# Optimization experiments

Hardware: AMD Instinct MI355X
Metric: run time of the kernel (lower is better)

Reference implementation:

```python
import jax, jax.numpy as jnp
import numpy as np

N_LAYERS = 32
HIDDEN = 1024
INTER = 2816
BATCH = 256
INIT_SCALE = 0.02


def setup_inputs() -> dict:
    key = jax.random.key(0)
    k_h, k_g, k_u, k_d = jax.random.split(key, 4)
    down_std = INIT_SCALE / np.sqrt(2 * N_LAYERS)
    h = jax.random.normal(k_h, (BATCH, N_LAYERS, HIDDEN), dtype=jnp.float32)
    # torch Linear weight layout: (out_features, in_features); stack over experts
    Wg = jax.random.normal(k_g, (N_LAYERS, INTER, HIDDEN), dtype=jnp.float32) * INIT_SCALE
    Wu = jax.random.normal(k_u, (N_LAYERS, INTER, HIDDEN), dtype=jnp.float32) * INIT_SCALE
    Wd = jax.random.normal(k_d, (N_LAYERS, HIDDEN, INTER), dtype=jnp.float32) * down_std
    return {"h": h, "Wg": Wg, "Wu": Wu, "Wd": Wd}


def reference(h, Wg, Wu, Wd):
    # h: (B, N, D); Wg/Wu: (N, I, D); Wd: (N, D, I)
    gate = jnp.einsum("bnd,nid->bni", h, Wg)
    up = jnp.einsum("bnd,nid->bni", h, Wu)
    act = jax.nn.silu(gate) * up            # (B, N, I)
    out = jnp.einsum("bni,ndi->bnd", act, Wd)  # (B, N, D)
    return out
```

## Files before the change

### kernel.cpp

```cpp
#include <hip/hip_runtime.h>
#include <hip/hip_bf16.h>

#define BATCH   256
#define NLAYERS 32
#define HID     1024
#define INTER   2816
#define BK      64

typedef __attribute__((ext_vector_type(8))) short bf16x8;
typedef __attribute__((ext_vector_type(4))) float f32x4;
typedef __attribute__((ext_vector_type(4))) int   i32x4;

__device__ __forceinline__ ushort f2bf(float f) {
  __hip_bfloat16 b = __float2bfloat16(f);
  return *reinterpret_cast<ushort*>(&b);
}

__device__ __forceinline__ bf16x8 cvt8(f32x4 a, f32x4 b) {
  bf16x8 o;
  o[0] = (short)f2bf(a[0]); o[1] = (short)f2bf(a[1]);
  o[2] = (short)f2bf(a[2]); o[3] = (short)f2bf(a[3]);
  o[4] = (short)f2bf(b[0]); o[5] = (short)f2bf(b[1]);
  o[6] = (short)f2bf(b[2]); o[7] = (short)f2bf(b[3]);
  return o;
}

__global__ __launch_bounds__(256) void k_pack(
    const float* __restrict__ h, ushort* __restrict__ Xp) {
  const int r    = blockIdx.x * 4 + (threadIdx.x >> 6);
  const int lane = threadIdx.x & 63;
  const int ro   = ((r & 31) * 256 + (r >> 5)) * 1024;
  const float* src = h + (size_t)r * 1024 + lane * 4;
  ushort* dst      = Xp + ro + lane * 4;
#pragma unroll
  for (int g = 0; g < 4; ++g) {
    f32x4 v = *(const f32x4*)(src + g * 256);
    ushort4 o;
    o.x = f2bf(v[0]); o.y = f2bf(v[1]); o.z = f2bf(v[2]); o.w = f2bf(v[3]);
    *(ushort4*)(dst + g * 256) = o;
  }
}

__global__ __launch_bounds__(512) void k_gateup(
    const ushort* __restrict__ Xp, const float* __restrict__ Wg,
    const float* __restrict__ Wu, ushort* __restrict__ act) {
  const int bid   = blockIdx.x;
  const int layer = bid / (INTER / 32);
  const int it    = bid % (INTER / 32);
  const int i0    = it * 32;
  const int tid   = threadIdx.x;
  const int lane  = tid & 63;
  const int wave  = tid >> 6;
  const int m0    = wave * 32;

  __shared__ ushort lds[BATCH * BK + 64 * BK];
  ushort* Al = lds;
  ushort* Wl = lds + BATCH * BK;

  f32x4 acc[2][4] = {};

  int aldst[4];
  const ushort* asrc[4];
#pragma unroll
  for (int r = 0; r < 4; ++r) {
    int g = tid + 512 * r;
    int arow = g >> 3, akc = g & 7;
    aldst[r] = arow * BK + ((akc ^ (arow & 7)) << 3);
    asrc[r] = Xp + ((size_t)layer * BATCH + arow) * HID + akc * 8;
  }
  const int wrow = tid >> 3, wsl = tid & 7;
  const int wldst = wrow * BK + ((wsl ^ (wrow & 7)) << 3);
  const float* wsrc = (wrow < 32 ? Wg + (size_t)(i0 + wrow) * HID
                                 : Wu + (size_t)(i0 + wrow - 32) * HID) +
                      (size_t)layer * INTER * HID + wsl * 8;

  i32x4 ra[4];
  f32x4 rw[2];
#pragma unroll
  for (int r = 0; r < 4; ++r) ra[r] = *(const i32x4*)asrc[r];
  rw[0] = *(const f32x4*)wsrc; rw[1] = *(const f32x4*)(wsrc + 4);

  const int r16 = lane & 15;
  const int g4  = lane >> 4;

  const int NK = HID / BK;
  for (int k = 0; k < NK; ++k) {
    __syncthreads();
#pragma unroll
    for (int r = 0; r < 4; ++r) *(i32x4*)&Al[aldst[r]] = ra[r];
    *(bf16x8*)&Wl[wldst] = cvt8(rw[0], rw[1]);
    __syncthreads();

    if (k + 1 < NK) {
      int off = (k + 1) * BK;
#pragma unroll
      for (int r = 0; r < 4; ++r) ra[r] = *(const i32x4*)(asrc[r] + off);
      rw[0] = *(const f32x4*)(wsrc + off); rw[1] = *(const f32x4*)(wsrc + off + 4);
    }

#pragma unroll
    for (int ks = 0; ks < 2; ++ks) {
      const int kg = ks * 4 + g4;
      bf16x8 af[2];
#pragma unroll
      for (int m = 0; m < 2; ++m) {
        int row = m0 + m * 16 + r16;
        af[m] = *(bf16x8*)&Al[row * BK + ((kg ^ (row & 7)) << 3)];
      }
#pragma unroll
      for (int n = 0; n < 4; ++n) {
        int row = n * 16 + r16;
        bf16x8 bw = *(bf16x8*)&Wl[row * BK + ((kg ^ (row & 7)) << 3)];
#pragma unroll
        for (int m = 0; m < 2; ++m)
          acc[m][n] = __builtin_amdgcn_mfma_f32_16x16x32_bf16(af[m], bw, acc[m][n], 0, 0, 0);
      }
    }
  }

  const int r4 = (lane >> 4) * 4;
#pragma unroll
  for (int m = 0; m < 2; ++m)
#pragma unroll
    for (int n = 0; n < 2; ++n)
#pragma unroll
      for (int r = 0; r < 4; ++r) {
        float g = acc[m][n][r];
        float u = acc[m][n + 2][r];
        float a = (g / (1.f + __expf(-g))) * u;
        int b = m0 + m * 16 + r4 + r;
        int i = i0 + n * 16 + r16;
        act[((size_t)layer * BATCH + b) * INTER + i] = f2bf(a);
      }
}

__global__ __launch_bounds__(512) void k_down(
    const ushort* __restrict__ act, const float* __restrict__ Wd,
    float* __restrict__ out) {
  const int bid   = blockIdx.x;
  const int layer = bid / (HID / 64);
  const int dtile = bid % (HID / 64);
  const int d0    = dtile * 64;
  const int tid   = threadIdx.x;
  const int lane  = tid & 63;
  const int wave  = tid >> 6;
  const int wm    = wave >> 1;
  const int wn    = wave & 1;

  __shared__ ushort lds[BATCH * BK + 64 * BK];
  ushort* Al = lds;
  ushort* Wl = lds + BATCH * BK;

  f32x4 acc[4][2] = {};

  int aldst[4];
  const ushort* asrc[4];
#pragma unroll
  for (int r = 0; r < 4; ++r) {
    int g = tid + 512 * r;
    int arow = g >> 3, akc = g & 7;
    aldst[r] = arow * BK + ((akc ^ (arow & 7)) << 3);
    asrc[r] = act + ((size_t)layer * BATCH + arow) * INTER + akc * 8;
  }
  const int wrow = tid >> 3, wkc = tid & 7;
  const int wldst = wrow * BK + ((wkc ^ (wrow & 7)) << 3);
  const float* wsrc = Wd + (size_t)layer * HID * INTER + (size_t)(d0 + wrow) * INTER + wkc * 8;

  i32x4 ra[4];
  f32x4 rw[2];

#pragma unroll
  for (int r = 0; r < 4; ++r) ra[r] = *(const i32x4*)asrc[r];
  rw[0] = *(const f32x4*)wsrc; rw[1] = *(const f32x4*)(wsrc + 4);

  const int NK = INTER / BK;
  for (int k = 0; k < NK; ++k) {
    __syncthreads();
#pragma unroll
    for (int r = 0; r < 4; ++r) *(i32x4*)&Al[aldst[r]] = ra[r];
    *(bf16x8*)&Wl[wldst] = cvt8(rw[0], rw[1]);
    __syncthreads();

    if (k + 1 < NK) {
      int off = (k + 1) * BK;
#pragma unroll
      for (int r = 0; r < 4; ++r) ra[r] = *(const i32x4*)(asrc[r] + off);
      rw[0] = *(const f32x4*)(wsrc + off); rw[1] = *(const f32x4*)(wsrc + off + 4);
    }

#pragma unroll
    for (int ks = 0; ks < 2; ++ks) {
      const int kg = ks * 4 + (lane >> 4);
      bf16x8 af[4];
#pragma unroll
      for (int m = 0; m < 4; ++m) {
        int row = wm * 64 + m * 16 + (lane & 15);
        af[m] = *(bf16x8*)&Al[row * BK + ((kg ^ (row & 7)) << 3)];
      }
#pragma unroll
      for (int n = 0; n < 2; ++n) {
        int row = wn * 32 + n * 16 + (lane & 15);
        bf16x8 bw = *(bf16x8*)&Wl[row * BK + ((kg ^ (row & 7)) << 3)];
#pragma unroll
        for (int m = 0; m < 4; ++m)
          acc[m][n] = __builtin_amdgcn_mfma_f32_16x16x32_bf16(af[m], bw, acc[m][n], 0, 0, 0);
      }
    }
  }

  const int c16 = lane & 15;
  const int r4  = (lane >> 4) * 4;
#pragma unroll
  for (int m = 0; m < 4; ++m)
#pragma unroll
    for (int n = 0; n < 2; ++n)
#pragma unroll
      for (int r = 0; r < 4; ++r) {
        int b = wm * 64 + m * 16 + r4 + r;
        int d = d0 + wn * 32 + n * 16 + c16;
        out[(size_t)b * (NLAYERS * HID) + (size_t)layer * HID + d] = acc[m][n][r];
      }
}

extern "C" void kernel_launch(void* const* d_in, const int* in_sizes, int n_in,
                              void* d_out, int out_size, void* d_ws, size_t ws_size,
                              hipStream_t stream) {
  const float* h  = (const float*)d_in[0];
  const float* Wg = (const float*)d_in[1];
  const float* Wu = (const float*)d_in[2];
  const float* Wd = (const float*)d_in[3];
  float* out  = (float*)d_out;
  ushort* act = (ushort*)d_ws;
  ushort* Xp  = (ushort*)d_ws + (size_t)NLAYERS * BATCH * INTER;

  hipLaunchKernelGGL(k_pack, dim3(BATCH * NLAYERS / 4), dim3(256), 0, stream,
                     h, Xp);
  hipLaunchKernelGGL(k_gateup, dim3(NLAYERS * (INTER / 32)), dim3(512), 0, stream,
                     Xp, Wg, Wu, act);
  hipLaunchKernelGGL(k_down, dim3(NLAYERS * (HID / 64)), dim3(512), 0, stream,
                     act, Wd, out);
}
```

Baseline: 329.0 us.

## Widen gate/up tile to 64 intermediate columns with 4x2 wave grid

The gate/up kernel now computes 64 intermediate columns per block instead of 32, staging 64 gate and 64 up weight rows in LDS. Waves are arranged as a 4x2 grid, each owning 64 batch rows by 32 columns for both gate and up. The aim is to halve redundant loads of the activation tile per layer and raise MFMA work per LDS read. In exchange the block uses more LDS and registers (16 accumulators), and the grid has half as many blocks. A launch-bounds occupancy hint is also added.

```diff
diff --git a/kernel.cpp b/kernel.cpp
--- a/kernel.cpp
+++ b/kernel.cpp
@@ -41,23 +41,24 @@
   }
 }
 
-__global__ __launch_bounds__(512) void k_gateup(
+__global__ __launch_bounds__(512, 4) void k_gateup(
     const ushort* __restrict__ Xp, const float* __restrict__ Wg,
     const float* __restrict__ Wu, ushort* __restrict__ act) {
   const int bid   = blockIdx.x;
-  const int layer = bid / (INTER / 32);
-  const int it    = bid % (INTER / 32);
-  const int i0    = it * 32;
+  const int layer = bid / (INTER / 64);
+  const int it    = bid % (INTER / 64);
+  const int i0    = it * 64;
   const int tid   = threadIdx.x;
   const int lane  = tid & 63;
   const int wave  = tid >> 6;
-  const int m0    = wave * 32;
-
-  __shared__ ushort lds[BATCH * BK + 64 * BK];
+  const int wm    = wave >> 1;
+  const int wn    = wave & 1;
+
+  __shared__ ushort lds[BATCH * BK + 128 * BK];
   ushort* Al = lds;
   ushort* Wl = lds + BATCH * BK;
 
-  f32x4 acc[2][4] = {};
+  f32x4 acc[4][2][2] = {};
 
   int aldst[4];
   const ushort* asrc[4];
@@ -69,16 +70,18 @@
     asrc[r] = Xp + ((size_t)layer * BATCH + arow) * HID + akc * 8;
   }
   const int wrow = tid >> 3, wsl = tid & 7;
-  const int wldst = wrow * BK + ((wsl ^ (wrow & 7)) << 3);
-  const float* wsrc = (wrow < 32 ? Wg + (size_t)(i0 + wrow) * HID
-                                 : Wu + (size_t)(i0 + wrow - 32) * HID) +
-                      (size_t)layer * INTER * HID + wsl * 8;
+  const int wldstG = wrow * BK + ((wsl ^ (wrow & 7)) << 3);
+  const int wrowU  = 64 + wrow;
+  const int wldstU = wrowU * BK + ((wsl ^ (wrowU & 7)) << 3);
+  const float* gsrc = Wg + (size_t)layer * INTER * HID + (size_t)(i0 + wrow) * HID + wsl * 8;
+  const float* usrc = Wu + (size_t)layer * INTER * HID + (size_t)(i0 + wrow) * HID + wsl * 8;
 
   i32x4 ra[4];
-  f32x4 rw[2];
+  f32x4 rg[2], ru[2];
 #pragma unroll
   for (int r = 0; r < 4; ++r) ra[r] = *(const i32x4*)asrc[r];
-  rw[0] = *(const f32x4*)wsrc; rw[1] = *(const f32x4*)(wsrc + 4);
+  rg[0] = *(const f32x4*)gsrc; rg[1] = *(const f32x4*)(gsrc + 4);
+  ru[0] = *(const f32x4*)usrc; ru[1] = *(const f32x4*)(usrc + 4);
 
   const int r16 = lane & 15;
   const int g4  = lane >> 4;
@@ -88,48 +91,54 @@
     __syncthreads();
 #pragma unroll
     for (int r = 0; r < 4; ++r) *(i32x4*)&Al[aldst[r]] = ra[r];
-    *(bf16x8*)&Wl[wldst] = cvt8(rw[0], rw[1]);
+    *(bf16x8*)&Wl[wldstG] = cvt8(rg[0], rg[1]);
+    *(bf16x8*)&Wl[wldstU] = cvt8(ru[0], ru[1]);
     __syncthreads();
 
     if (k + 1 < NK) {
       int off = (k + 1) * BK;
 #pragma unroll
       for (int r = 0; r < 4; ++r) ra[r] = *(const i32x4*)(asrc[r] + off);
-      rw[0] = *(const f32x4*)(wsrc + off); rw[1] = *(const f32x4*)(wsrc + off + 4);
+      rg[0] = *(const f32x4*)(gsrc + off); rg[1] = *(const f32x4*)(gsrc + off + 4);
+      ru[0] = *(const f32x4*)(usrc + off); ru[1] = *(const f32x4*)(usrc + off + 4);
     }
 
 #pragma unroll
     for (int ks = 0; ks < 2; ++ks) {
       const int kg = ks * 4 + g4;
-      bf16x8 af[2];
-#pragma unroll
-      for (int m = 0; m < 2; ++m) {
-        int row = m0 + m * 16 + r16;
+      bf16x8 af[4];
+#pragma unroll
+      for (int m = 0; m < 4; ++m) {
+        int row = wm * 64 + m * 16 + r16;
         af[m] = *(bf16x8*)&Al[row * BK + ((kg ^ (row & 7)) << 3)];
       }
 #pragma unroll
-      for (int n = 0; n < 4; ++n) {
-        int row = n * 16 + r16;
-        bf16x8 bw = *(bf16x8*)&Wl[row * BK + ((kg ^ (row & 7)) << 3)];
-#pragma unroll
-        for (int m = 0; m < 2; ++m)
-          acc[m][n] = __builtin_amdgcn_mfma_f32_16x16x32_bf16(af[m], bw, acc[m][n], 0, 0, 0);
+      for (int n = 0; n < 2; ++n) {
+        int rowG = wn * 32 + n * 16 + r16;
+        int rowU = 64 + rowG;
+        bf16x8 bg = *(bf16x8*)&Wl[rowG * BK + ((kg ^ (rowG & 7)) << 3)];
+        bf16x8 bu = *(bf16x8*)&Wl[rowU * BK + ((kg ^ (rowU & 7)) << 3)];
+#pragma unroll
+        for (int m = 0; m < 4; ++m) {
+          acc[m][n][0] = __builtin_amdgcn_mfma_f32_16x16x32_bf16(af[m], bg, acc[m][n][0], 0, 0, 0);
+          acc[m][n][1] = __builtin_amdgcn_mfma_f32_16x16x32_bf16(af[m], bu, acc[m][n][1], 0, 0, 0);
+        }
       }
     }
   }
 
   const int r4 = (lane >> 4) * 4;
 #pragma unroll
-  for (int m = 0; m < 2; ++m)
+  for (int m = 0; m < 4; ++m)
 #pragma unroll
     for (int n = 0; n < 2; ++n)
 #pragma unroll
       for (int r = 0; r < 4; ++r) {
-        float g = acc[m][n][r];
-        float u = acc[m][n + 2][r];
+        float g = acc[m][n][0][r];
+        float u = acc[m][n][1][r];
         float a = (g / (1.f + __expf(-g))) * u;
-        int b = m0 + m * 16 + r4 + r;
-        int i = i0 + n * 16 + r16;
+        int b = wm * 64 + m * 16 + r4 + r;
+        int i = i0 + wn * 32 + n * 16 + r16;
         act[((size_t)layer * BATCH + b) * INTER + i] = f2bf(a);
       }
 }
@@ -235,7 +244,7 @@
 
   hipLaunchKernelGGL(k_pack, dim3(BATCH * NLAYERS / 4), dim3(256), 0, stream,
                      h, Xp);
-  hipLaunchKernelGGL(k_gateup, dim3(NLAYERS * (INTER / 32)), dim3(512), 0, stream,
+  hipLaunchKernelGGL(k_gateup, dim3(NLAYERS * (INTER / 64)), dim3(512), 0, stream,
                      Xp, Wg, Wu, act);
   hipLaunchKernelGGL(k_down, dim3(NLAYERS * (HID / 64)), dim3(512), 0, stream,
                      act, Wd, out);
```

Result: slower. 337.5 us (+2.6%).

## Keep activation rows in registers for gate/up GEMM, stage only weights in LDS

Applied to the files above, without the earlier changes.

The gate/up kernel now loads each wave's 16 batch rows across the full hidden dimension into registers once. Only the gate and up weight tiles are staged through LDS, so the activation tile no longer has to be copied through shared memory on every K step. Blocks grow to 1024 threads, and each block covers 64 intermediate columns in two passes of 32. The catch is heavy register use (128 VGPRs just for A fragments) together with an aggressive launch bound, which risks spills or low occupancy. Only half the threads stage weights, and there are still two barriers per K step.

```diff
diff --git a/kernel.cpp b/kernel.cpp
--- a/kernel.cpp
+++ b/kernel.cpp
@@ -25,7 +25,7 @@
   return o;
 }
 
-__global__ __launch_bounds__(256) void k_pack(
+__global__ __launch_bounds__(256) void k_pack_v3(
     const float* __restrict__ h, ushort* __restrict__ Xp) {
   const int r    = blockIdx.x * 4 + (threadIdx.x >> 6);
   const int lane = threadIdx.x & 63;
@@ -41,100 +41,84 @@
   }
 }
 
-__global__ __launch_bounds__(512) void k_gateup(
+__global__ __launch_bounds__(1024, 8) void k_gateup_reg(
     const ushort* __restrict__ Xp, const float* __restrict__ Wg,
     const float* __restrict__ Wu, ushort* __restrict__ act) {
   const int bid   = blockIdx.x;
-  const int layer = bid / (INTER / 32);
-  const int it    = bid % (INTER / 32);
-  const int i0    = it * 32;
+  const int layer = bid / 44;
+  const int i0    = (bid % 44) * 64;
   const int tid   = threadIdx.x;
   const int lane  = tid & 63;
   const int wave  = tid >> 6;
-  const int m0    = wave * 32;
-
-  __shared__ ushort lds[BATCH * BK + 64 * BK];
-  ushort* Al = lds;
-  ushort* Wl = lds + BATCH * BK;
-
-  f32x4 acc[2][4] = {};
-
-  int aldst[4];
-  const ushort* asrc[4];
-#pragma unroll
-  for (int r = 0; r < 4; ++r) {
-    int g = tid + 512 * r;
-    int arow = g >> 3, akc = g & 7;
-    aldst[r] = arow * BK + ((akc ^ (arow & 7)) << 3);
-    asrc[r] = Xp + ((size_t)layer * BATCH + arow) * HID + akc * 8;
-  }
-  const int wrow = tid >> 3, wsl = tid & 7;
-  const int wldst = wrow * BK + ((wsl ^ (wrow & 7)) << 3);
-  const float* wsrc = (wrow < 32 ? Wg + (size_t)(i0 + wrow) * HID
-                                 : Wu + (size_t)(i0 + wrow - 32) * HID) +
-                      (size_t)layer * INTER * HID + wsl * 8;
-
-  i32x4 ra[4];
-  f32x4 rw[2];
-#pragma unroll
-  for (int r = 0; r < 4; ++r) ra[r] = *(const i32x4*)asrc[r];
-  rw[0] = *(const f32x4*)wsrc; rw[1] = *(const f32x4*)(wsrc + 4);
-
-  const int r16 = lane & 15;
-  const int g4  = lane >> 4;
-
-  const int NK = HID / BK;
-  for (int k = 0; k < NK; ++k) {
-    __syncthreads();
-#pragma unroll
-    for (int r = 0; r < 4; ++r) *(i32x4*)&Al[aldst[r]] = ra[r];
-    *(bf16x8*)&Wl[wldst] = cvt8(rw[0], rw[1]);
-    __syncthreads();
-
-    if (k + 1 < NK) {
-      int off = (k + 1) * BK;
-#pragma unroll
-      for (int r = 0; r < 4; ++r) ra[r] = *(const i32x4*)(asrc[r] + off);
-      rw[0] = *(const f32x4*)(wsrc + off); rw[1] = *(const f32x4*)(wsrc + off + 4);
+  const int r16   = lane & 15;
+  const int g4    = lane >> 4;
+
+  __shared__ ushort Wl[64 * 64];
+
+  bf16x8 a[32];
+  {
+    const ushort* ap = Xp + ((size_t)layer * BATCH + wave * 16 + r16) * HID + g4 * 8;
+#pragma unroll
+    for (int s = 0; s < 32; ++s)
+      a[s] = *(const bf16x8*)(ap + s * 32);
+  }
+
+  const bool stg  = (tid < 512);
+  const int  wrow = (tid & 511) >> 3;
+  const int  wsl  = tid & 7;
+  const int  wldst = wrow * 64 + ((wsl ^ (wrow & 7)) << 3);
+
+#pragma unroll
+  for (int pass = 0; pass < 2; ++pass) {
+    const int ip = i0 + pass * 32;
+    const float* wsrc = (wrow < 32 ? Wg + (size_t)(ip + wrow) * HID
+                                   : Wu + (size_t)(ip + wrow - 32) * HID)
+                        + (size_t)layer * INTER * HID + wsl * 8;
+    f32x4 rw0, rw1;
+    if (stg) { rw0 = *(const f32x4*)wsrc; rw1 = *(const f32x4*)(wsrc + 4); }
+
+    f32x4 acc[2][2] = {};
+
+#pragma unroll
+    for (int k = 0; k < 16; ++k) {
+      __syncthreads();
+      if (stg) *(bf16x8*)&Wl[wldst] = cvt8(rw0, rw1);
+      __syncthreads();
+      if (k < 15 && stg) {
+        rw0 = *(const f32x4*)(wsrc + (k + 1) * 64);
+        rw1 = *(const f32x4*)(wsrc + (k + 1) * 64 + 4);
+      }
+#pragma unroll
+      for (int ks = 0; ks < 2; ++ks) {
+        const int kg = ks * 4 + g4;
+#pragma unroll
+        for (int n = 0; n < 2; ++n) {
+          const int rg_ = n * 16 + r16;
+          const int ru_ = 32 + rg_;
+          bf16x8 bg = *(bf16x8*)&Wl[rg_ * 64 + ((kg ^ (rg_ & 7)) << 3)];
+          bf16x8 bu = *(bf16x8*)&Wl[ru_ * 64 + ((kg ^ (ru_ & 7)) << 3)];
+          acc[n][0] = __builtin_amdgcn_mfma_f32_16x16x32_bf16(a[2 * k + ks], bg, acc[n][0], 0, 0, 0);
+          acc[n][1] = __builtin_amdgcn_mfma_f32_16x16x32_bf16(a[2 * k + ks], bu, acc[n][1], 0, 0, 0);
+        }
+      }
     }
 
-#pragma unroll
-    for (int ks = 0; ks < 2; ++ks) {
-      const int kg = ks * 4 + g4;
-      bf16x8 af[2];
-#pragma unroll
-      for (int m = 0; m < 2; ++m) {
-        int row = m0 + m * 16 + r16;
-        af[m] = *(bf16x8*)&Al[row * BK + ((kg ^ (row & 7)) << 3)];
-      }
-#pragma unroll
-      for (int n = 0; n < 4; ++n) {
-        int row = n * 16 + r16;
-        bf16x8 bw = *(bf16x8*)&Wl[row * BK + ((kg ^ (row & 7)) << 3)];
-#pragma unroll
-        for (int m = 0; m < 2; ++m)
-          acc[m][n] = __builtin_amdgcn_mfma_f32_16x16x32_bf16(af[m], bw, acc[m][n], 0, 0, 0);
-      }
-    }
-  }
-
-  const int r4 = (lane >> 4) * 4;
-#pragma unroll
-  for (int m = 0; m < 2; ++m)
+    const int r4 = g4 * 4;
 #pragma unroll
     for (int n = 0; n < 2; ++n)
 #pragma unroll
       for (int r = 0; r < 4; ++r) {
-        float g = acc[m][n][r];
-        float u = acc[m][n + 2][r];
-        float a = (g / (1.f + __expf(-g))) * u;
-        int b = m0 + m * 16 + r4 + r;
-        int i = i0 + n * 16 + r16;
-        act[((size_t)layer * BATCH + b) * INTER + i] = f2bf(a);
-      }
-}
-
-__global__ __launch_bounds__(512) void k_down(
+        float g = acc[n][0][r];
+        float u = acc[n][1][r];
+        float v = (g / (1.f + __expf(-g))) * u;
+        int b = wave * 16 + r4 + r;
+        int i = ip + n * 16 + r16;
+        act[((size_t)layer * BATCH + b) * INTER + i] = f2bf(v);
+      }
+  }
+}
+
+__global__ __launch_bounds__(512) void k_down_v3(
     const ushort* __restrict__ act, const float* __restrict__ Wd,
     float* __restrict__ out) {
   const int bid   = blockIdx.x;
@@ -233,10 +217,10 @@
   ushort* act = (ushort*)d_ws;
   ushort* Xp  = (ushort*)d_ws + (size_t)NLAYERS * BATCH * INTER;
 
-  hipLaunchKernelGGL(k_pack, dim3(BATCH * NLAYERS / 4), dim3(256), 0, stream,
+  hipLaunchKernelGGL(k_pack_v3, dim3(BATCH * NLAYERS / 4), dim3(256), 0, stream,
                      h, Xp);
-  hipLaunchKernelGGL(k_gateup, dim3(NLAYERS * (INTER / 32)), dim3(512), 0, stream,
+  hipLaunchKernelGGL(k_gateup_reg, dim3(NLAYERS * (INTER / 64)), dim3(1024), 0, stream,
                      Xp, Wg, Wu, act);
-  hipLaunchKernelGGL(k_down, dim3(NLAYERS * (HID / 64)), dim3(512), 0, stream,
+  hipLaunchKernelGGL(k_down_v3, dim3(NLAYERS * (HID / 64)), dim3(512), 0, stream,
                      act, Wd, out);
 }
```

Result: slower. 710.9 us (+116.1%).
